# Performance work log

Hardware: AMD Instinct MI355X
Metric: run time of the kernel (lower is better)

Reference implementation:

```python
import jax, jax.numpy as jnp
import numpy as np

N = 100000

def _gcn_norm(edge_index, n):
    row, col = edge_index[0], edge_index[1]
    deg = jnp.zeros((n,), jnp.float32).at[col].add(1.0)
    dinv = jnp.where(deg > 0, jax.lax.rsqrt(jnp.maximum(deg, 1.0)), 0.0)
    return dinv[row] * dinv[col]


def _arma_conv(x, row, col, norm, init_w, w, root_w, bias):
    # x: [N, Fin]; init_w: [K, Fin, F]; w: [T-1, K, F, F]; root_w: [T, K, Fin, F]; bias: [T, K, 1, F]
    out = jnp.einsum('nf,kfg->kng', x, init_w)  # [K, N, F]
    T = root_w.shape[0]
    for t in range(T):
        if t > 0:
            out = jnp.einsum('kng,kgh->knh', out, w[t - 1])
        msg = out[:, row, :] * norm[None, :, None]          # [K, E, F] gather
        out = jnp.zeros_like(out).at[:, col, :].add(msg)    # scatter-add to targets
        out = out + jnp.einsum('nf,kfg->kng', x, root_w[t]) + bias[t]
        out = jax.nn.relu(out)
    return out.mean(axis=0)  # average over stacks K


def setup_inputs() -> dict:
    key = jax.random.key(0)
    ks = jax.random.split(key, 12)
    E, Fin, H, C, K = 1600000, 128, 64, 41, 2
    s = 0.1
    return {
        'x': jax.random.normal(ks[0], (N, Fin), jnp.float32),
        'edge_index': jax.random.randint(ks[1], (2, E), 0, N, jnp.int64),
        'w1_init': jax.random.normal(ks[2], (K, Fin, H), jnp.float32) * s,
        'w1': jax.random.normal(ks[3], (1, K, H, H), jnp.float32) * s,
        'w1_root': jax.random.normal(ks[4], (2, K, Fin, H), jnp.float32) * s,
        'b1': jax.random.normal(ks[5], (2, K, 1, H), jnp.float32) * s,
        'w2_init': jax.random.normal(ks[6], (K, H, C), jnp.float32) * s,
        'w2': jax.random.normal(ks[7], (1, K, C, C), jnp.float32) * s,
        'w2_root': jax.random.normal(ks[8], (2, K, H, C), jnp.float32) * s,
        'b2': jax.random.normal(ks[9], (2, K, 1, C), jnp.float32) * s,
    }


def reference(x, edge_index, w1_init, w1, w1_root, b1, w2_init, w2, w2_root, b2):
    row, col = edge_index[0], edge_index[1]
    norm = _gcn_norm(edge_index, N)
    h = jax.nn.relu(_arma_conv(x, row, col, norm, w1_init, w1, w1_root, b1))
    # F.dropout is identity in eval mode
    h = _arma_conv(h, row, col, norm, w2_init, w2, w2_root, b2)
    return jax.nn.log_softmax(h, axis=1)
```

## Files before the change

### kernel.cpp

```cpp
#include <hip/hip_runtime.h>
#include <math.h>

#define TPB 256
typedef unsigned short ushort_t;
typedef unsigned int uint_t;
typedef __attribute__((ext_vector_type(8))) short bf16x8;
typedef __attribute__((ext_vector_type(4))) float f32x4;

__device__ __forceinline__ float bf2f(ushort_t h) {
    return __uint_as_float(((uint_t)h) << 16);
}
__device__ __forceinline__ ushort_t f2bf(float f) {
    uint_t u = __float_as_uint(f);
    u += 0x7fff + ((u >> 16) & 1);
    return (ushort_t)(u >> 16);
}
__device__ __forceinline__ uint_t pack2(float x, float y) {
    return (uint_t)f2bf(x) | ((uint_t)f2bf(y) << 16);
}

__global__ void rank_kernel(const int* __restrict__ col, int* __restrict__ cnt,
                            int* __restrict__ pos, int E) {
    int e = blockIdx.x * blockDim.x + threadIdx.x;
    if (e < E) pos[e] = atomicAdd(&cnt[col[e]], 1);
}

__global__ void dinv_kernel(const int* __restrict__ cnt, float* __restrict__ dinv, int n) {
    int i = blockIdx.x * blockDim.x + threadIdx.x;
    if (i < n) {
        int d = cnt[i];
        dinv[i] = (d > 0) ? rsqrtf((float)d) : 0.0f;
    }
}

__global__ void scan_block(const int* __restrict__ cnt, int* __restrict__ incl,
                           int* __restrict__ bsum, int N) {
    __shared__ int s[TPB];
    int i = blockIdx.x * TPB + threadIdx.x;
    s[threadIdx.x] = (i < N) ? cnt[i] : 0;
    __syncthreads();
    for (int d = 1; d < TPB; d <<= 1) {
        int t = (threadIdx.x >= d) ? s[threadIdx.x - d] : 0;
        __syncthreads();
        s[threadIdx.x] += t;
        __syncthreads();
    }
    if (i < N) incl[i] = s[threadIdx.x];
    if (threadIdx.x == TPB - 1) bsum[blockIdx.x] = s[TPB - 1];
}

__global__ void scan_bsums(int* __restrict__ bsum, int nb) {
    __shared__ int s[512];
    int t = threadIdx.x;
    int v = (t < nb) ? bsum[t] : 0;
    s[t] = v;
    __syncthreads();
    for (int d = 1; d < 512; d <<= 1) {
        int u = (t >= d) ? s[t - d] : 0;
        __syncthreads();
        s[t] += u;
        __syncthreads();
    }
    if (t < nb) bsum[t] = s[t] - v;
}

__global__ void finalize_csr(const int* __restrict__ incl, const int* __restrict__ bsum,
                             int* __restrict__ rowstart, int N) {
    int i = blockIdx.x * TPB + threadIdx.x;
    if (i < N) rowstart[i + 1] = incl[i] + bsum[blockIdx.x];
    if (i == 0) rowstart[0] = 0;
}

__global__ void fill_csr(const int* __restrict__ row, const int* __restrict__ col,
                         const int* __restrict__ rowstart, const int* __restrict__ pos,
                         int* __restrict__ srcidx, int E) {
    int e = blockIdx.x * blockDim.x + threadIdx.x;
    if (e < E) srcidx[rowstart[col[e]] + pos[e]] = row[e];
}

__global__ void cvt4_kernel(const float4* __restrict__ src, uint2* __restrict__ dst, int n4) {
    int i = blockIdx.x * blockDim.x + threadIdx.x;
    if (i < n4) {
        float4 v = src[i];
        dst[i] = make_uint2(pack2(v.x, v.y), pack2(v.z, v.w));
    }
}

#define SWZ_A 32768
#define SWZ_B 24576
#define SWZ_C 12288
#define SWZ_D 12288
__global__ void swz_all(const float* __restrict__ w1_init, const float* __restrict__ w1,
                        const float* __restrict__ w1_root, const float* __restrict__ w2_init,
                        const float* __restrict__ w2, const float* __restrict__ w2_root,
                        short* __restrict__ dst) {
    int idx = blockIdx.x * blockDim.x + threadIdx.x;
    int region, base, CH, CT;
    if (idx < SWZ_A)                          { region = 0; base = 0; CH = 4; CT = 8; }
    else if (idx < SWZ_A + SWZ_B)             { region = 1; base = SWZ_A; CH = 6; CT = 4; }
    else if (idx < SWZ_A + SWZ_B + SWZ_C)     { region = 2; base = SWZ_A + SWZ_B; CH = 2; CT = 6; }
    else if (idx < SWZ_A + SWZ_B + SWZ_C + SWZ_D)
                                              { region = 3; base = SWZ_A + SWZ_B + SWZ_C; CH = 4; CT = 3; }
    else return;
    int r = idx - base;
    int j = r & 7, ln = (r >> 3) & 63;
    int rest = r >> 9;
    int ct = rest % CT, c = (rest / CT) % CH, k = rest / (CT * CH);
    int col = ct * 16 + (ln & 15);
    int kl = (ln >> 4) * 8 + j;
    float v = 0.0f;
    if (region == 0) {
        int kk = c * 32 + kl;
        if (col < 64)       v = w1_init[((size_t)k * 128 + kk) * 64 + col];
        else                v = w1_root[((size_t)(0 * 2 + k) * 128 + kk) * 64 + (col - 64)];
    } else if (region == 1) {
        if (c < 2) { int kk = c * 32 + kl;        v = w1[((size_t)k * 64 + kk) * 64 + col]; }
        else       { int kk = (c - 2) * 32 + kl;  v = w1_root[((size_t)(2 + k) * 128 + kk) * 64 + col]; }
    } else if (region == 2) {
        int kk = c * 32 + kl;
        if (col < 48) { if (col < 41)            v = w2_init[((size_t)k * 64 + kk) * 41 + col]; }
        else          { int c2 = col - 48; if (c2 < 41) v = w2_root[((size_t)(0 * 2 + k) * 64 + kk) * 41 + c2]; }
    } else {
        if (c < 2) { int kk = c * 32 + kl;       if (kk < 41 && col < 41) v = w2[((size_t)k * 41 + kk) * 41 + col]; }
        else       { int kk = (c - 2) * 32 + kl; if (col < 41)            v = w2_root[((size_t)(2 + k) * 64 + kk) * 41 + col]; }
    }
    dst[(size_t)base + r] = (short)f2bf(v);
}

template<int CT, int CTA, int CH>
__global__ __launch_bounds__(256)
void gemm_t0(const ushort_t* __restrict__ s2, int s2s, const short* __restrict__ fragbuf,
             const float* __restrict__ biasB, int FB, int N,
             float* __restrict__ pre, ushort_t* __restrict__ outH) {
    const int k = blockIdx.y;
    const int n0 = blockIdx.x * 128;
    const int t = threadIdx.x;
    const int w = t >> 6, lane = t & 63, quad = lane >> 4, lr = lane & 15;
    const short* fb = fragbuf + (size_t)k * CH * CT * 512;

    int r0 = n0 + w * 32 + lr;
    int m0 = r0 < N ? r0 : N - 1;
    int m1 = (r0 + 16) < N ? (r0 + 16) : N - 1;

    f32x4 acc[2][CT];
#pragma unroll
    for (int rt = 0; rt < 2; ++rt)
#pragma unroll
        for (int ct = 0; ct < CT; ++ct) acc[rt][ct] = (f32x4){0.f, 0.f, 0.f, 0.f};

#pragma unroll
    for (int c = 0; c < CH; ++c) {
        int off = c * 32 + quad * 8;
        bf16x8 a0 = *(const bf16x8*)&s2[(size_t)m0 * s2s + off];
        bf16x8 a1 = *(const bf16x8*)&s2[(size_t)m1 * s2s + off];
#pragma unroll
        for (int ct = 0; ct < CT; ++ct) {
            bf16x8 b = *(const bf16x8*)&fb[((size_t)c * CT + ct) * 512 + lane * 8];
            acc[0][ct] = __builtin_amdgcn_mfma_f32_16x16x32_bf16(a0, b, acc[0][ct], 0, 0, 0);
            acc[1][ct] = __builtin_amdgcn_mfma_f32_16x16x32_bf16(a1, b, acc[1][ct], 0, 0, 0);
        }
    }

    const int FWB = (CT - CTA) * 16;
#pragma unroll
    for (int rt = 0; rt < 2; ++rt) {
#pragma unroll
        for (int i = 0; i < 4; ++i) {
            int n = n0 + w * 32 + rt * 16 + quad * 4 + i;
            if (n >= N) continue;
#pragma unroll
            for (int ct = 0; ct < CT; ++ct) {
                int col = ct * 16 + lr;
                float v = acc[rt][ct][i];
                if (ct < CTA) {
                    outH[((size_t)n * 2 + k) * (CTA * 16) + col] = f2bf(v);
                } else {
                    int c2 = col - CTA * 16;
                    if (c2 < FB) v += biasB[(size_t)k * FB + c2];
                    pre[((size_t)k * N + n) * FWB + c2] = v;
                }
            }
        }
    }
}

__global__ __launch_bounds__(256)
void gemm_t1_l1(const ushort_t* __restrict__ s1, const ushort_t* __restrict__ xh,
                const short* __restrict__ fragbuf, const float* __restrict__ bias ,
                int N, ushort_t* __restrict__ hh) {
    constexpr int CT = 4, CH = 6;
    const int n0 = blockIdx.x * 128;
    const int t = threadIdx.x;
    const int w = t >> 6, lane = t & 63, quad = lane >> 4, lr = lane & 15;

    int r0 = n0 + w * 32 + lr;
    int m0 = r0 < N ? r0 : N - 1;
    int m1 = (r0 + 16) < N ? (r0 + 16) : N - 1;

    f32x4 acc[2][2][CT];
#pragma unroll
    for (int k = 0; k < 2; ++k)
#pragma unroll
        for (int rt = 0; rt < 2; ++rt)
#pragma unroll
            for (int ct = 0; ct < CT; ++ct) acc[k][rt][ct] = (f32x4){0.f, 0.f, 0.f, 0.f};

#pragma unroll
    for (int c = 0; c < CH; ++c) {
        bf16x8 a0[2], a1[2];
        if (c < 2) {
            int off = c * 32 + quad * 8;
#pragma unroll
            for (int k = 0; k < 2; ++k) {
                a0[k] = *(const bf16x8*)&s1[((size_t)m0 * 2 + k) * 64 + off];
                a1[k] = *(const bf16x8*)&s1[((size_t)m1 * 2 + k) * 64 + off];
            }
        } else {
            int off = (c - 2) * 32 + quad * 8;
            a0[0] = a0[1] = *(const bf16x8*)&xh[(size_t)m0 * 128 + off];
            a1[0] = a1[1] = *(const bf16x8*)&xh[(size_t)m1 * 128 + off];
        }
#pragma unroll
        for (int k = 0; k < 2; ++k) {
            const short* fb = fragbuf + (size_t)k * CH * CT * 512;
#pragma unroll
            for (int ct = 0; ct < CT; ++ct) {
                bf16x8 b = *(const bf16x8*)&fb[((size_t)c * CT + ct) * 512 + lane * 8];
                acc[k][0][ct] = __builtin_amdgcn_mfma_f32_16x16x32_bf16(a0[k], b, acc[k][0][ct], 0, 0, 0);
                acc[k][1][ct] = __builtin_amdgcn_mfma_f32_16x16x32_bf16(a1[k], b, acc[k][1][ct], 0, 0, 0);
            }
        }
    }

#pragma unroll
    for (int rt = 0; rt < 2; ++rt) {
#pragma unroll
        for (int i = 0; i < 4; ++i) {
            int n = n0 + w * 32 + rt * 16 + quad * 4 + i;
            if (n >= N) continue;
#pragma unroll
            for (int ct = 0; ct < CT; ++ct) {
                int col = ct * 16 + lr;
                float v0 = fmaxf(acc[0][rt][ct][i] + bias[col], 0.0f);
                float v1 = fmaxf(acc[1][rt][ct][i] + bias[64 + col], 0.0f);
                hh[(size_t)n * 64 + col] = f2bf(0.5f * (v0 + v1));
            }
        }
    }
}

__global__ __launch_bounds__(256)
void gemm_t1_l2(const ushort_t* __restrict__ s1, const ushort_t* __restrict__ hh,
                const short* __restrict__ fragbuf, const float* __restrict__ bias ,
                int N, float* __restrict__ out) {
    constexpr int CT = 3, CH = 4;
    const int n0 = blockIdx.x * 128;
    const int t = threadIdx.x;
    const int w = t >> 6, lane = t & 63, quad = lane >> 4, lr = lane & 15;

    int r0 = n0 + w * 32 + lr;
    int m0 = r0 < N ? r0 : N - 1;
    int m1 = (r0 + 16) < N ? (r0 + 16) : N - 1;

    f32x4 acc[2][2][CT];
#pragma unroll
    for (int k = 0; k < 2; ++k)
#pragma unroll
        for (int rt = 0; rt < 2; ++rt)
#pragma unroll
            for (int ct = 0; ct < CT; ++ct) acc[k][rt][ct] = (f32x4){0.f, 0.f, 0.f, 0.f};

#pragma unroll
    for (int c = 0; c < CH; ++c) {
        bf16x8 a0[2], a1[2];
        if (c < 2) {
            int off = c * 32 + quad * 8;
#pragma unroll
            for (int k = 0; k < 2; ++k) {
                a0[k] = *(const bf16x8*)&s1[((size_t)m0 * 2 + k) * 48 + off];
                a1[k] = *(const bf16x8*)&s1[((size_t)m1 * 2 + k) * 48 + off];
            }
        } else {
            int off = (c - 2) * 32 + quad * 8;
            a0[0] = a0[1] = *(const bf16x8*)&hh[(size_t)m0 * 64 + off];
            a1[0] = a1[1] = *(const bf16x8*)&hh[(size_t)m1 * 64 + off];
        }
#pragma unroll
        for (int k = 0; k < 2; ++k) {
            const short* fb = fragbuf + (size_t)k * CH * CT * 512;
#pragma unroll
            for (int ct = 0; ct < CT; ++ct) {
                bf16x8 b = *(const bf16x8*)&fb[((size_t)c * CT + ct) * 512 + lane * 8];
                acc[k][0][ct] = __builtin_amdgcn_mfma_f32_16x16x32_bf16(a0[k], b, acc[k][0][ct], 0, 0, 0);
                acc[k][1][ct] = __builtin_amdgcn_mfma_f32_16x16x32_bf16(a1[k], b, acc[k][1][ct], 0, 0, 0);
            }
        }
    }

#pragma unroll
    for (int rt = 0; rt < 2; ++rt) {
#pragma unroll
        for (int i = 0; i < 4; ++i) {
            int n = n0 + w * 32 + rt * 16 + quad * 4 + i;
            float m[CT];
            float mx = -1e30f;
#pragma unroll
            for (int ct = 0; ct < CT; ++ct) {
                int col = ct * 16 + lr;
                float b0 = (col < 41) ? bias[col] : 0.0f;
                float b1v = (col < 41) ? bias[41 + col] : 0.0f;
                float v0 = fmaxf(acc[0][rt][ct][i] + b0, 0.0f);
                float v1 = fmaxf(acc[1][rt][ct][i] + b1v, 0.0f);
                m[ct] = 0.5f * (v0 + v1);
                if (col < 41) mx = fmaxf(mx, m[ct]);
            }
#pragma unroll
            for (int msk = 1; msk < 16; msk <<= 1) mx = fmaxf(mx, __shfl_xor(mx, msk));
            float s = 0.0f;
#pragma unroll
            for (int ct = 0; ct < CT; ++ct) {
                int col = ct * 16 + lr;
                if (col < 41) s += __expf(m[ct] - mx);
            }
#pragma unroll
            for (int msk = 1; msk < 16; msk <<= 1) s += __shfl_xor(s, msk);
            float ls = __logf(s);
            if (n < N) {
#pragma unroll
                for (int ct = 0; ct < CT; ++ct) {
                    int col = ct * 16 + lr;
                    if (col < 41) out[(size_t)n * 41 + col] = m[ct] - mx - ls;
                }
            }
        }
    }
}

template<int PAIRS>
__global__ __launch_bounds__(256)
void gather(const int* __restrict__ rowstart, const int* __restrict__ srcidx,
            const float* __restrict__ dinv, const uint_t* __restrict__ msg,
            const float* __restrict__ pre, uint_t* __restrict__ outH, int FW, int N) {
    int gt = blockIdx.x * 256 + threadIdx.x;
    int n = gt >> 6, lane = gt & 63;
    if (n >= N) return;
    int k, pair;
    if (PAIRS == 32) { k = lane >> 5; pair = lane & 31; }
    else { k = lane / PAIRS; pair = lane - k * PAIRS; }
    if (k >= 2) return;
    int beg = rowstart[n], end = rowstart[n + 1];
    float dn = dinv[n];
    float ax = 0.0f, ay = 0.0f;
    int e = beg;
    for (; e + 3 < end; e += 4) {
        int s0 = srcidx[e], s1 = srcidx[e + 1], s2 = srcidx[e + 2], s3 = srcidx[e + 3];
        float w0 = dinv[s0] * dn, w1 = dinv[s1] * dn, w2 = dinv[s2] * dn, w3 = dinv[s3] * dn;
        uint_t u0 = msg[((size_t)s0 * 2 + k) * PAIRS + pair];
        uint_t u1 = msg[((size_t)s1 * 2 + k) * PAIRS + pair];
        uint_t u2 = msg[((size_t)s2 * 2 + k) * PAIRS + pair];
        uint_t u3 = msg[((size_t)s3 * 2 + k) * PAIRS + pair];
        ax = fmaf(bf2f((ushort_t)u0), w0, ax);
        ay = fmaf(bf2f((ushort_t)(u0 >> 16)), w0, ay);
        ax = fmaf(bf2f((ushort_t)u1), w1, ax);
        ay = fmaf(bf2f((ushort_t)(u1 >> 16)), w1, ay);
        ax = fmaf(bf2f((ushort_t)u2), w2, ax);
        ay = fmaf(bf2f((ushort_t)(u2 >> 16)), w2, ay);
        ax = fmaf(bf2f((ushort_t)u3), w3, ax);
        ay = fmaf(bf2f((ushort_t)(u3 >> 16)), w3, ay);
    }
    for (; e < end; ++e) {
        int s0 = srcidx[e];
        float w0 = dinv[s0] * dn;
        uint_t u0 = msg[((size_t)s0 * 2 + k) * PAIRS + pair];
        ax = fmaf(bf2f((ushort_t)u0), w0, ax);
        ay = fmaf(bf2f((ushort_t)(u0 >> 16)), w0, ay);
    }
    size_t oidx = ((size_t)n * 2 + k) * PAIRS + pair;
    if (pre) {
        const float* p = &pre[((size_t)k * N + n) * FW + 2 * pair];
        outH[oidx] = pack2(fmaxf(p[0] + ax, 0.0f), fmaxf(p[1] + ay, 0.0f));
    } else {
        outH[oidx] = pack2(ax, ay);
    }
}

extern "C" void kernel_launch(void* const* d_in, const int* in_sizes, int n_in,
                              void* d_out, int out_size, void* d_ws, size_t ws_size,
                              hipStream_t stream) {
    const float* x       = (const float*)d_in[0];
    const int*   ei      = (const int*)  d_in[1];
    const float* w1_init = (const float*)d_in[2];
    const float* w1      = (const float*)d_in[3];
    const float* w1_root = (const float*)d_in[4];
    const float* b1      = (const float*)d_in[5];
    const float* w2_init = (const float*)d_in[6];
    const float* w2      = (const float*)d_in[7];
    const float* w2_root = (const float*)d_in[8];
    const float* b2      = (const float*)d_in[9];

    const int Fin1 = 128;
    int N = in_sizes[0] / Fin1;
    int E = in_sizes[1] / 2;
    const int* row = ei;
    const int* col = ei + E;

    char* ws = (char*)d_ws;
    size_t off = 0;
    auto carve = [&](size_t bytes) -> void* {
        void* p = ws + off;
        off += (bytes + 255) & ~(size_t)255;
        return p;
    };
    int nblkN = (N + TPB - 1) / TPB;
    int*      cnt      = (int*)     carve((size_t)N * 4);
    int*      incl     = (int*)     carve((size_t)N * 4);
    int*      rowstart = (int*)     carve((size_t)(N + 1) * 4);
    int*      bsum     = (int*)     carve((size_t)nblkN * 4);
    float*    dinv     = (float*)   carve((size_t)N * 4);
    int*      pos      = (int*)     carve((size_t)E * 4);
    int*      srcidx   = (int*)     carve((size_t)E * 4);
    short*    swz      = (short*)   carve((size_t)(SWZ_A + SWZ_B + SWZ_C + SWZ_D) * 2);
    ushort_t* xh       = (ushort_t*)carve((size_t)N * 128 * 2);
    ushort_t* hh       = (ushort_t*)carve((size_t)N * 64 * 2);
    ushort_t* b16A     = (ushort_t*)carve((size_t)N * 2 * 64 * 2);
    ushort_t* b16B     = (ushort_t*)carve((size_t)N * 2 * 64 * 2);
    float*    pre      = (float*)   carve((size_t)2 * N * 64 * 4);

    hipMemsetAsync(cnt, 0, (size_t)N * 4, stream);
    rank_kernel <<<(E + TPB - 1) / TPB, TPB, 0, stream>>>(col, cnt, pos, E);
    dinv_kernel <<<nblkN, TPB, 0, stream>>>(cnt, dinv, N);
    scan_block  <<<nblkN, TPB, 0, stream>>>(cnt, incl, bsum, N);
    scan_bsums  <<<1, 512, 0, stream>>>(bsum, nblkN);
    finalize_csr<<<nblkN, TPB, 0, stream>>>(incl, bsum, rowstart, N);
    fill_csr    <<<(E + TPB - 1) / TPB, TPB, 0, stream>>>(row, col, rowstart, pos, srcidx, E);

    int swztot = SWZ_A + SWZ_B + SWZ_C + SWZ_D;
    swz_all<<<(swztot + TPB - 1) / TPB, TPB, 0, stream>>>(w1_init, w1, w1_root,
                                                          w2_init, w2, w2_root, swz);
    int nx4 = N * 128 / 4;
    cvt4_kernel<<<(nx4 + TPB - 1) / TPB, TPB, 0, stream>>>((const float4*)x, (uint2*)xh, nx4);

    dim3 gg2((N + 127) / 128, 2);
    dim3 gg1((N + 127) / 128, 1);
    int ggb = (N * 64 + TPB - 1) / TPB;
    const short* swzA = swz;
    const short* swzB = swz + SWZ_A;
    const short* swzC = swz + SWZ_A + SWZ_B;
    const short* swzD = swz + SWZ_A + SWZ_B + SWZ_C;

    gemm_t0<8, 4, 4><<<gg2, TPB, 0, stream>>>(xh, 128, swzA, b1, 64, N, pre, b16A);
    gather<32><<<ggb, TPB, 0, stream>>>(rowstart, srcidx, dinv, (const uint_t*)b16A,
                                        pre, (uint_t*)b16B, 64, N);
    gather<32><<<ggb, TPB, 0, stream>>>(rowstart, srcidx, dinv, (const uint_t*)b16B,
                                        nullptr, (uint_t*)b16A, 64, N);
    gemm_t1_l1<<<gg1, TPB, 0, stream>>>(b16A, xh, swzB, b1 + 2 * 64, N, hh);

    gemm_t0<6, 3, 2><<<gg2, TPB, 0, stream>>>(hh, 64, swzC, b2, 41, N, pre, b16A);
    gather<24><<<ggb, TPB, 0, stream>>>(rowstart, srcidx, dinv, (const uint_t*)b16A,
                                        pre, (uint_t*)b16B, 48, N);
    gather<24><<<ggb, TPB, 0, stream>>>(rowstart, srcidx, dinv, (const uint_t*)b16B,
                                        nullptr, (uint_t*)b16A, 48, N);
    gemm_t1_l2<<<gg1, TPB, 0, stream>>>(b16A, hh, swzD, b2 + 2 * 41, N, (float*)d_out);
}
```

Baseline: 630.0 us.

## Pack bf16 pairs on GEMM output, store pre in bf16, split-edge vectorized gather

```diff
diff --git a/kernel.cpp b/kernel.cpp
--- a/kernel.cpp
+++ b/kernel.cpp
@@ -23,14 +23,6 @@
                             int* __restrict__ pos, int E) {
     int e = blockIdx.x * blockDim.x + threadIdx.x;
     if (e < E) pos[e] = atomicAdd(&cnt[col[e]], 1);
-}
-
-__global__ void dinv_kernel(const int* __restrict__ cnt, float* __restrict__ dinv, int n) {
-    int i = blockIdx.x * blockDim.x + threadIdx.x;
-    if (i < n) {
-        int d = cnt[i];
-        dinv[i] = (d > 0) ? rsqrtf((float)d) : 0.0f;
-    }
 }
 
 __global__ void scan_block(const int* __restrict__ cnt, int* __restrict__ incl,
@@ -65,9 +57,14 @@
 }
 
 __global__ void finalize_csr(const int* __restrict__ incl, const int* __restrict__ bsum,
-                             int* __restrict__ rowstart, int N) {
+                             const int* __restrict__ cnt, int* __restrict__ rowstart,
+                             float* __restrict__ dinv, int N) {
     int i = blockIdx.x * TPB + threadIdx.x;
-    if (i < N) rowstart[i + 1] = incl[i] + bsum[blockIdx.x];
+    if (i < N) {
+        rowstart[i + 1] = incl[i] + bsum[blockIdx.x];
+        int d = cnt[i];
+        dinv[i] = (d > 0) ? rsqrtf((float)d) : 0.0f;
+    }
     if (i == 0) rowstart[0] = 0;
 }
 
@@ -112,14 +109,14 @@
     if (region == 0) {
         int kk = c * 32 + kl;
         if (col < 64)       v = w1_init[((size_t)k * 128 + kk) * 64 + col];
-        else                v = w1_root[((size_t)(0 * 2 + k) * 128 + kk) * 64 + (col - 64)];
+        else                v = w1_root[((size_t)k * 128 + kk) * 64 + (col - 64)];
     } else if (region == 1) {
         if (c < 2) { int kk = c * 32 + kl;        v = w1[((size_t)k * 64 + kk) * 64 + col]; }
         else       { int kk = (c - 2) * 32 + kl;  v = w1_root[((size_t)(2 + k) * 128 + kk) * 64 + col]; }
     } else if (region == 2) {
         int kk = c * 32 + kl;
         if (col < 48) { if (col < 41)            v = w2_init[((size_t)k * 64 + kk) * 41 + col]; }
-        else          { int c2 = col - 48; if (c2 < 41) v = w2_root[((size_t)(0 * 2 + k) * 64 + kk) * 41 + c2]; }
+        else          { int c2 = col - 48; if (c2 < 41) v = w2_root[((size_t)k * 64 + kk) * 41 + c2]; }
     } else {
         if (c < 2) { int kk = c * 32 + kl;       if (kk < 41 && col < 41) v = w2[((size_t)k * 41 + kk) * 41 + col]; }
         else       { int kk = (c - 2) * 32 + kl; if (col < 41)            v = w2_root[((size_t)(2 + k) * 64 + kk) * 41 + col]; }
@@ -131,7 +128,9 @@
 __global__ __launch_bounds__(256)
 void gemm_t0(const ushort_t* __restrict__ s2, int s2s, const short* __restrict__ fragbuf,
              const float* __restrict__ biasB, int FB, int N,
-             float* __restrict__ pre, ushort_t* __restrict__ outH) {
+             uint_t* __restrict__ pre, uint_t* __restrict__ outH) {
+    constexpr int PP = (CT - CTA) * 8;
+    constexpr int PA = CTA * 8;
     const int k = blockIdx.y;
     const int n0 = blockIdx.x * 128;
     const int t = threadIdx.x;
@@ -161,7 +160,6 @@
         }
     }
 
-    const int FWB = (CT - CTA) * 16;
 #pragma unroll
     for (int rt = 0; rt < 2; ++rt) {
 #pragma unroll
@@ -173,11 +171,15 @@
                 int col = ct * 16 + lr;
                 float v = acc[rt][ct][i];
                 if (ct < CTA) {
-                    outH[((size_t)n * 2 + k) * (CTA * 16) + col] = f2bf(v);
+                    float vn = __shfl_xor(v, 1);
+                    if (!(lr & 1))
+                        outH[((size_t)n * 2 + k) * PA + (col >> 1)] = pack2(v, vn);
                 } else {
                     int c2 = col - CTA * 16;
                     if (c2 < FB) v += biasB[(size_t)k * FB + c2];
-                    pre[((size_t)k * N + n) * FWB + c2] = v;
+                    float vn = __shfl_xor(v, 1);
+                    if (!(lr & 1))
+                        pre[((size_t)n * 2 + k) * PP + (c2 >> 1)] = pack2(v, vn);
                 }
             }
         }
@@ -186,8 +188,8 @@
 
 __global__ __launch_bounds__(256)
 void gemm_t1_l1(const ushort_t* __restrict__ s1, const ushort_t* __restrict__ xh,
-                const short* __restrict__ fragbuf, const float* __restrict__ bias ,
-                int N, ushort_t* __restrict__ hh) {
+                const short* __restrict__ fragbuf, const float* __restrict__ bias,
+                int N, uint_t* __restrict__ hhU) {
     constexpr int CT = 4, CH = 6;
     const int n0 = blockIdx.x * 128;
     const int t = threadIdx.x;
@@ -243,7 +245,9 @@
                 int col = ct * 16 + lr;
                 float v0 = fmaxf(acc[0][rt][ct][i] + bias[col], 0.0f);
                 float v1 = fmaxf(acc[1][rt][ct][i] + bias[64 + col], 0.0f);
-                hh[(size_t)n * 64 + col] = f2bf(0.5f * (v0 + v1));
+                float m = 0.5f * (v0 + v1);
+                float mn = __shfl_xor(m, 1);
+                if (!(lr & 1)) hhU[(size_t)n * 32 + (col >> 1)] = pack2(m, mn);
             }
         }
     }
@@ -251,7 +255,7 @@
 
 __global__ __launch_bounds__(256)
 void gemm_t1_l2(const ushort_t* __restrict__ s1, const ushort_t* __restrict__ hh,
-                const short* __restrict__ fragbuf, const float* __restrict__ bias ,
+                const short* __restrict__ fragbuf, const float* __restrict__ bias,
                 int N, float* __restrict__ out) {
     constexpr int CT = 3, CH = 4;
     const int n0 = blockIdx.x * 128;
@@ -338,49 +342,58 @@
 
 template<int PAIRS>
 __global__ __launch_bounds__(256)
-void gather(const int* __restrict__ rowstart, const int* __restrict__ srcidx,
-            const float* __restrict__ dinv, const uint_t* __restrict__ msg,
-            const float* __restrict__ pre, uint_t* __restrict__ outH, int FW, int N) {
+void gather2(const int* __restrict__ rowstart, const int* __restrict__ srcidx,
+             const float* __restrict__ dinv, const uint_t* __restrict__ msg,
+             const uint_t* __restrict__ pre, uint_t* __restrict__ outH, int N) {
     int gt = blockIdx.x * 256 + threadIdx.x;
     int n = gt >> 6, lane = gt & 63;
     if (n >= N) return;
-    int k, pair;
-    if (PAIRS == 32) { k = lane >> 5; pair = lane & 31; }
-    else { k = lane / PAIRS; pair = lane - k * PAIRS; }
-    if (k >= 2) return;
+    const int es = lane / PAIRS;
+    const int u = lane % PAIRS;
     int beg = rowstart[n], end = rowstart[n + 1];
     float dn = dinv[n];
-    float ax = 0.0f, ay = 0.0f;
-    int e = beg;
-    for (; e + 3 < end; e += 4) {
-        int s0 = srcidx[e], s1 = srcidx[e + 1], s2 = srcidx[e + 2], s3 = srcidx[e + 3];
-        float w0 = dinv[s0] * dn, w1 = dinv[s1] * dn, w2 = dinv[s2] * dn, w3 = dinv[s3] * dn;
-        uint_t u0 = msg[((size_t)s0 * 2 + k) * PAIRS + pair];
-        uint_t u1 = msg[((size_t)s1 * 2 + k) * PAIRS + pair];
-        uint_t u2 = msg[((size_t)s2 * 2 + k) * PAIRS + pair];
-        uint_t u3 = msg[((size_t)s3 * 2 + k) * PAIRS + pair];
-        ax = fmaf(bf2f((ushort_t)u0), w0, ax);
-        ay = fmaf(bf2f((ushort_t)(u0 >> 16)), w0, ay);
-        ax = fmaf(bf2f((ushort_t)u1), w1, ax);
-        ay = fmaf(bf2f((ushort_t)(u1 >> 16)), w1, ay);
-        ax = fmaf(bf2f((ushort_t)u2), w2, ax);
-        ay = fmaf(bf2f((ushort_t)(u2 >> 16)), w2, ay);
-        ax = fmaf(bf2f((ushort_t)u3), w3, ax);
-        ay = fmaf(bf2f((ushort_t)(u3 >> 16)), w3, ay);
-    }
-    for (; e < end; ++e) {
-        int s0 = srcidx[e];
-        float w0 = dinv[s0] * dn;
-        uint_t u0 = msg[((size_t)s0 * 2 + k) * PAIRS + pair];
-        ax = fmaf(bf2f((ushort_t)u0), w0, ax);
-        ay = fmaf(bf2f((ushort_t)(u0 >> 16)), w0, ay);
-    }
-    size_t oidx = ((size_t)n * 2 + k) * PAIRS + pair;
-    if (pre) {
-        const float* p = &pre[((size_t)k * N + n) * FW + 2 * pair];
-        outH[oidx] = pack2(fmaxf(p[0] + ax, 0.0f), fmaxf(p[1] + ay, 0.0f));
-    } else {
-        outH[oidx] = pack2(ax, ay);
+    float a0 = 0.f, a1 = 0.f, a2 = 0.f, a3 = 0.f;
+    if (es < 2) {
+        int e = beg + es;
+        for (; e + 2 < end; e += 4) {
+            int s0 = srcidx[e], s1 = srcidx[e + 2];
+            float w0 = dinv[s0] * dn, w1 = dinv[s1] * dn;
+            uint2 m0 = *(const uint2*)&msg[(size_t)s0 * (2 * PAIRS) + 2 * u];
+            uint2 m1 = *(const uint2*)&msg[(size_t)s1 * (2 * PAIRS) + 2 * u];
+            a0 = fmaf(bf2f((ushort_t)m0.x), w0, a0);
+            a1 = fmaf(bf2f((ushort_t)(m0.x >> 16)), w0, a1);
+            a2 = fmaf(bf2f((ushort_t)m0.y), w0, a2);
+            a3 = fmaf(bf2f((ushort_t)(m0.y >> 16)), w0, a3);
+            a0 = fmaf(bf2f((ushort_t)m1.x), w1, a0);
+            a1 = fmaf(bf2f((ushort_t)(m1.x >> 16)), w1, a1);
+            a2 = fmaf(bf2f((ushort_t)m1.y), w1, a2);
+            a3 = fmaf(bf2f((ushort_t)(m1.y >> 16)), w1, a3);
+        }
+        if (e < end) {
+            int s0 = srcidx[e];
+            float w0 = dinv[s0] * dn;
+            uint2 m0 = *(const uint2*)&msg[(size_t)s0 * (2 * PAIRS) + 2 * u];
+            a0 = fmaf(bf2f((ushort_t)m0.x), w0, a0);
+            a1 = fmaf(bf2f((ushort_t)(m0.x >> 16)), w0, a1);
+            a2 = fmaf(bf2f((ushort_t)m0.y), w0, a2);
+            a3 = fmaf(bf2f((ushort_t)(m0.y >> 16)), w0, a3);
+        }
+    }
+    float b0 = __shfl(a0, u + PAIRS);
+    float b1 = __shfl(a1, u + PAIRS);
+    float b2 = __shfl(a2, u + PAIRS);
+    float b3 = __shfl(a3, u + PAIRS);
+    if (lane < PAIRS) {
+        a0 += b0; a1 += b1; a2 += b2; a3 += b3;
+        size_t o = (size_t)n * (2 * PAIRS) + 2 * u;
+        if (pre) {
+            uint2 p = *(const uint2*)&pre[o];
+            a0 = fmaxf(a0 + bf2f((ushort_t)p.x), 0.f);
+            a1 = fmaxf(a1 + bf2f((ushort_t)(p.x >> 16)), 0.f);
+            a2 = fmaxf(a2 + bf2f((ushort_t)p.y), 0.f);
+            a3 = fmaxf(a3 + bf2f((ushort_t)(p.y >> 16)), 0.f);
+        }
+        *(uint2*)&outH[o] = make_uint2(pack2(a0, a1), pack2(a2, a3));
     }
 }
 
@@ -424,14 +437,13 @@
     ushort_t* hh       = (ushort_t*)carve((size_t)N * 64 * 2);
     ushort_t* b16A     = (ushort_t*)carve((size_t)N * 2 * 64 * 2);
     ushort_t* b16B     = (ushort_t*)carve((size_t)N * 2 * 64 * 2);
-    float*    pre      = (float*)   carve((size_t)2 * N * 64 * 4);
+    uint_t*   pre      = (uint_t*)  carve((size_t)N * 2 * 32 * 4);
 
     hipMemsetAsync(cnt, 0, (size_t)N * 4, stream);
     rank_kernel <<<(E + TPB - 1) / TPB, TPB, 0, stream>>>(col, cnt, pos, E);
-    dinv_kernel <<<nblkN, TPB, 0, stream>>>(cnt, dinv, N);
     scan_block  <<<nblkN, TPB, 0, stream>>>(cnt, incl, bsum, N);
     scan_bsums  <<<1, 512, 0, stream>>>(bsum, nblkN);
-    finalize_csr<<<nblkN, TPB, 0, stream>>>(incl, bsum, rowstart, N);
+    finalize_csr<<<nblkN, TPB, 0, stream>>>(incl, bsum, cnt, rowstart, dinv, N);
     fill_csr    <<<(E + TPB - 1) / TPB, TPB, 0, stream>>>(row, col, rowstart, pos, srcidx, E);
 
     int swztot = SWZ_A + SWZ_B + SWZ_C + SWZ_D;
@@ -448,17 +460,17 @@
     const short* swzC = swz + SWZ_A + SWZ_B;
     const short* swzD = swz + SWZ_A + SWZ_B + SWZ_C;
 
-    gemm_t0<8, 4, 4><<<gg2, TPB, 0, stream>>>(xh, 128, swzA, b1, 64, N, pre, b16A);
-    gather<32><<<ggb, TPB, 0, stream>>>(rowstart, srcidx, dinv, (const uint_t*)b16A,
-                                        pre, (uint_t*)b16B, 64, N);
-    gather<32><<<ggb, TPB, 0, stream>>>(rowstart, srcidx, dinv, (const uint_t*)b16B,
-                                        nullptr, (uint_t*)b16A, 64, N);
-    gemm_t1_l1<<<gg1, TPB, 0, stream>>>(b16A, xh, swzB, b1 + 2 * 64, N, hh);
-
-    gemm_t0<6, 3, 2><<<gg2, TPB, 0, stream>>>(hh, 64, swzC, b2, 41, N, pre, b16A);
-    gather<24><<<ggb, TPB, 0, stream>>>(rowstart, srcidx, dinv, (const uint_t*)b16A,
-                                        pre, (uint_t*)b16B, 48, N);
-    gather<24><<<ggb, TPB, 0, stream>>>(rowstart, srcidx, dinv, (const uint_t*)b16B,
-                                        nullptr, (uint_t*)b16A, 48, N);
+    gemm_t0<8, 4, 4><<<gg2, TPB, 0, stream>>>(xh, 128, swzA, b1, 64, N, pre, (uint_t*)b16A);
+    gather2<32><<<ggb, TPB, 0, stream>>>(rowstart, srcidx, dinv, (const uint_t*)b16A,
+                                         pre, (uint_t*)b16B, N);
+    gather2<32><<<ggb, TPB, 0, stream>>>(rowstart, srcidx, dinv, (const uint_t*)b16B,
+                                         nullptr, (uint_t*)b16A, N);
+    gemm_t1_l1<<<gg1, TPB, 0, stream>>>(b16A, xh, swzB, b1 + 2 * 64, N, (uint_t*)hh);
+
+    gemm_t0<6, 3, 2><<<gg2, TPB, 0, stream>>>(hh, 64, swzC, b2, 41, N, pre, (uint_t*)b16A);
+    gather2<24><<<ggb, TPB, 0, stream>>>(rowstart, srcidx, dinv, (const uint_t*)b16A,
+                                         pre, (uint_t*)b16B, N);
+    gather2<24><<<ggb, TPB, 0, stream>>>(rowstart, srcidx, dinv, (const uint_t*)b16B,
+                                         nullptr, (uint_t*)b16A, N);
     gemm_t1_l2<<<gg1, TPB, 0, stream>>>(b16A, hh, swzD, b2 + 2 * 41, N, (float*)d_out);
 }
```

Measured after the change: 700.6 us. 11.2% more time.
